# Kernel tuning notes

Hardware: AMD Instinct MI355X
Metric: run time of the kernel (lower is better)

## Reference

```python
import jax, jax.numpy as jnp
import numpy as np

D_MODEL = 1024
NUM_HEADS = 16
HEAD_DIM = D_MODEL // NUM_HEADS


def setup_inputs() -> dict:
    key = jax.random.key(0)
    k_x, k_wqkv, k_bqkv, k_wo, k_bo = jax.random.split(key, 5)
    B, T = 4, 2048
    s = 1.0 / np.sqrt(D_MODEL)
    return {
        "x": jax.random.normal(k_x, (B, T, D_MODEL), dtype=jnp.float32),
        "w_qkv": jax.random.uniform(k_wqkv, (D_MODEL, 3 * D_MODEL), jnp.float32, -s, s),
        "b_qkv": jax.random.uniform(k_bqkv, (3 * D_MODEL,), jnp.float32, -s, s),
        "w_out": jax.random.uniform(k_wo, (D_MODEL, D_MODEL), jnp.float32, -s, s),
        "b_out": jax.random.uniform(k_bo, (D_MODEL,), jnp.float32, -s, s),
    }


def reference(x, w_qkv, b_qkv, w_out, b_out):
    B, T, _ = x.shape
    H, Dh = NUM_HEADS, HEAD_DIM
    scale = Dh ** -0.5
    qkv = x @ w_qkv + b_qkv                       # [B,T,3D]
    qkv = qkv.reshape(B, T, 3, H, Dh)
    q = jnp.transpose(qkv[:, :, 0], (0, 2, 1, 3))  # [B,H,T,Dh]
    k = jnp.transpose(qkv[:, :, 1], (0, 2, 1, 3))
    v = jnp.transpose(qkv[:, :, 2], (0, 2, 1, 3))
    scores = jnp.einsum('bhqd,bhkd->bhqk', q, k) * scale
    causal = jnp.tril(jnp.ones((T, T), dtype=bool))
    scores = jnp.where(causal, scores, -jnp.inf)
    w = jax.nn.softmax(scores, axis=-1)
    out = jnp.einsum('bhqk,bhkd->bhqd', w, v)     # [B,H,T,Dh]
    out = jnp.transpose(out, (0, 2, 1, 3)).reshape(B, T, H * Dh)
    return out @ w_out + b_out
```

## Files before the change

kernel.cpp:

```cpp
#include <hip/hip_runtime.h>

typedef unsigned short u16;
typedef unsigned u32;
typedef float f32x4 __attribute__((ext_vector_type(4)));
typedef __bf16 bf16x8 __attribute__((ext_vector_type(8)));
typedef __bf16 bf16x2 __attribute__((ext_vector_type(2)));
typedef u32 u32x4 __attribute__((ext_vector_type(4)));
typedef u16 u16x4 __attribute__((ext_vector_type(4)));
typedef int i32x2 __attribute__((ext_vector_type(2)));

#define MFMA_16x16x32(a, b, c) __builtin_amdgcn_mfma_f32_16x16x32_bf16((a), (b), (c), 0, 0, 0)

#if __has_builtin(__builtin_amdgcn_exp2f)
#define EXP2(x) __builtin_amdgcn_exp2f(x)
#else
#define EXP2(x) exp2f(x)
#endif


__device__ __forceinline__ u16 f2bf(float f) {
  unsigned u = __builtin_bit_cast(unsigned, f);
  unsigned r = ((u >> 16) & 1u) + 0x7FFFu;
  return (u16)((u + r) >> 16);
}

__device__ __forceinline__ u32 pk2(float x, float y) {
  bf16x2 v = {(__bf16)x, (__bf16)y};
  return __builtin_bit_cast(u32, v);
}

__device__ __forceinline__ void gload16(const void* g, void* l) {
  __builtin_amdgcn_global_load_lds(
      (const __attribute__((address_space(1))) void*)g,
      (__attribute__((address_space(3))) void*)l, 16, 0, 0);
}



__global__ void cvt_to_bf16(const float* __restrict__ in, u16* __restrict__ out, int n) {
  const int s = blockIdx.x * 256 + threadIdx.x;
  if (s * 8 >= n) return;
  const int l = s & 63, f = (s >> 6) & 7, kb = (s >> 9) & 31, R = s >> 14;
  const int rr = ((f >> 2) << 6) + ((f & 3) << 4) + (l & 15);
  const int row = (R << 7) + rr;
  const int k = (kb << 5) + ((l >> 4) << 3);
  const float* src = in + (size_t)row * 1024 + k;
  const f32x4 a = *(const f32x4*)src;
  const f32x4 b = *(const f32x4*)(src + 4);
  u16x4 u0, u1;
#pragma unroll
  for (int j = 0; j < 4; ++j) { u0[j] = f2bf(a[j]); u1[j] = f2bf(b[j]); }
  *(u16x4*)(out + (size_t)s * 8) = u0;
  *(u16x4*)(out + (size_t)s * 8 + 4) = u1;
}

__global__ void transpose_cvt(const float* __restrict__ in, u16* __restrict__ out,
                              int rows, int cols) {
  __shared__ float t[64][65];
  const int rb = blockIdx.y * 64, cb = blockIdx.x * 64;
  for (int i = threadIdx.x; i < 4096; i += 256) {
    const int r = i >> 6, c = i & 63;
    t[r][c] = in[(size_t)(rb + r) * cols + cb + c];
  }
  __syncthreads();
  for (int u = threadIdx.x; u < 512; u += 256) {
    const int c = u >> 3, k8 = u & 7;
    const int nrow = cb + c;
    const int kg = rb + k8 * 8;
    const int R = nrow >> 7, rr = nrow & 127;
    const int fB = ((rr >> 6) << 2) + ((rr >> 4) & 3);
    const int kb = kg >> 5, koct = (kg >> 3) & 3;
    u16* dst = out + (((size_t)R * 32 + kb) * 8 + fB) * 512 + ((koct << 4) + (rr & 15)) * 8;
    u16x4 u0, u1;
#pragma unroll
    for (int j = 0; j < 4; ++j) {
      u0[j] = f2bf(t[k8 * 8 + j][c]);
      u1[j] = f2bf(t[k8 * 8 + 4 + j][c]);
    }
    *(u16x4*)dst = u0;
    *(u16x4*)(dst + 4) = u1;
  }
}

template <int EPI>
__global__ __launch_bounds__(256, 4) void gemm_bt(
    const u16* __restrict__ A, const u16* __restrict__ Bt, int K,
    const float* __restrict__ bias,
    u16* __restrict__ oq, u16* __restrict__ ok, u16* __restrict__ ov,
    float* __restrict__ of, int N, int nbx) {
  __shared__ __align__(16) u16 As[8192];
  __shared__ __align__(16) u16 Bs[8192];
  const int tid = threadIdx.x;
  const int lane = tid & 63, w = tid >> 6;
  const int g = lane >> 4, cc = lane & 15;
  const int wr = w >> 1, wc = w & 1;

  const int cpx = gridDim.x >> 3;
  const int bid = ((int)blockIdx.x & 7) * cpx + ((int)blockIdx.x >> 3);
  const int bx = bid % nbx, by = bid / nbx;

  const u16* pa = A + ((size_t)by * 256 + w) * 512 + lane * 8;
  const u16* pb = Bt + ((size_t)bx * 256 + w) * 512 + lane * 8;

  u16* la0 = &As[w * 512 + lane * 8];
  u16* lb0 = &Bs[w * 512 + lane * 8];
  const u16* ard = &As[(wr * 4) * 512 + lane * 8];
  const u16* brd = &Bs[(wc * 4) * 512 + lane * 8];

  f32x4 acc[4][4] = {};

  const int ns = K >> 6;
  for (int s = 0; s < ns; ++s) {
    const size_t o = (size_t)s * 8192;
    gload16(pa + o, la0);
    gload16(pa + o + 2048, la0 + 2048);
    gload16(pa + o + 4096, la0 + 4096);
    gload16(pa + o + 6144, la0 + 6144);
    gload16(pb + o, lb0);
    gload16(pb + o + 2048, lb0 + 2048);
    gload16(pb + o + 4096, lb0 + 4096);
    gload16(pb + o + 6144, lb0 + 6144);
    __syncthreads();
#pragma unroll
    for (int kk = 0; kk < 2; ++kk) {
      bf16x8 af[4], bf[4];
#pragma unroll
      for (int mi = 0; mi < 4; ++mi) af[mi] = *(const bf16x8*)(ard + kk * 4096 + mi * 512);
#pragma unroll
      for (int ni = 0; ni < 4; ++ni) bf[ni] = *(const bf16x8*)(brd + kk * 4096 + ni * 512);
      __builtin_amdgcn_s_setprio(1);
#pragma unroll
      for (int mi = 0; mi < 4; ++mi)
#pragma unroll
        for (int ni = 0; ni < 4; ++ni)
          acc[mi][ni] = MFMA_16x16x32(af[mi], bf[ni], acc[mi][ni]);
      __builtin_amdgcn_s_setprio(0);
    }
    __syncthreads();
  }

  const int m00 = by * 128 + wr * 64 + 4 * g;
  const int n00 = bx * 128 + wc * 64;
#pragma unroll
  for (int ni = 0; ni < 4; ++ni) {
    const int n = n00 + ni * 16 + cc;
    const float bn = bias[n];
    if constexpr (EPI == 0) {
      const int which = n >> 10;
      const int d = n & 1023;
      const int h = d >> 6, dh = d & 63;
      const int dcf = dh >> 5, gf = (dh >> 3) & 3, e = dh & 7;
      const int niv = dh >> 4, ccv = dh & 15;
#pragma unroll
      for (int mi = 0; mi < 4; ++mi) {
        const int mb = m00 + mi * 16;
        const int b = mb >> 11, t0b = mb & 2047;
        const int bh2 = b * 16 + h;
        const int kt = t0b >> 7, tr = t0b & 127;
        if (which == 2) {
          const int kk0 = (tr & ~12) | ((tr & 4) << 1) | ((tr & 8) >> 1);
          const int ko = kk0 >> 5, gv = (kk0 >> 3) & 3, ev = kk0 & 7;
          u16x4 pk;
#pragma unroll
          for (int r = 0; r < 4; ++r) pk[r] = f2bf(acc[mi][ni][r] + bn);
          *(u16x4*)&ov[(((size_t)bh2 * 16 + kt) * 16 + ko * 4 + niv) * 512 +
                       ((gv << 4) + ccv) * 8 + ev] = pk;
        } else if (which == 1) {
          const int ki = tr >> 4;
          u16* dst = ok + (((size_t)bh2 * 16 + kt) * 16 + dcf * 8 + ki) * 512 +
                     ((gf << 4) + (tr & 15)) * 8 + e;
#pragma unroll
          for (int r = 0; r < 4; ++r) dst[r * 8] = f2bf(acc[mi][ni][r] + bn);
        } else {
          const int wf = tr >> 5, mif = (tr >> 4) & 1;
          u16* dst = oq + (((size_t)bh2 * 16 + kt) * 16 + wf * 4 + mif * 2 + dcf) * 512 +
                     ((gf << 4) + (tr & 15)) * 8 + e;
#pragma unroll
          for (int r = 0; r < 4; ++r) dst[r * 8] = f2bf(acc[mi][ni][r] + bn);
        }
      }
    } else {
#pragma unroll
      for (int mi = 0; mi < 4; ++mi) {
        const int m = m00 + mi * 16;
#pragma unroll
        for (int r = 0; r < 4; ++r) of[(size_t)(m + r) * N + n] = acc[mi][ni][r] + bn;
      }
    }
  }
}

__global__ __launch_bounds__(256, 3) void flash_attn(
    const u16* __restrict__ Qb, const u16* __restrict__ Kb,
    const u16* __restrict__ Vt, u16* __restrict__ Ob) {
  __shared__ __align__(16) u16 Ks[8192];
  __shared__ __align__(16) u16 Vs[8192];

  const int bid = blockIdx.x;
  const int tq4 = bid >> 6, t0 = tq4 & 3, ti = tq4 >> 2;
  const int qt = (ti == 0) ? 15 - t0 : (ti == 1) ? 8 + t0 : (ti == 2) ? 7 - t0 : t0;
  const int bh = bid & 63;
  const int tid = threadIdx.x;
  const int lane = tid & 63, w = tid >> 6;
  const int g = lane >> 4, cc = lane & 15;
  const int q0 = qt * 128 + w * 32;

  bf16x8 bq[2][2];
  {
    const u16* qp = Qb + (((size_t)bh * 16 + qt) * 16 + w * 4) * 512 + lane * 8;
#pragma unroll
    for (int mi = 0; mi < 2; ++mi)
#pragma unroll
      for (int dc = 0; dc < 2; ++dc)
        bq[mi][dc] = *(const bf16x8*)(qp + (mi * 2 + dc) * 512);
  }

  const char* kp = (const char*)Kb + (size_t)bh * 262144 + w * 1024 + lane * 16;
  const char* vp = (const char*)Vt + (size_t)bh * 262144 + w * 1024 + lane * 16;
  u16* kl[4];
  u16* vl[4];
#pragma unroll
  for (int i = 0; i < 4; ++i) {
    kl[i] = &Ks[(i * 4 + w) * 512 + lane * 8];
    vl[i] = &Vs[(i * 4 + w) * 512 + lane * 8];
  }
  const u16* krd = &Ks[lane * 8];
  const u16* vrd = &Vs[lane * 8];

  const u32x4 ones_u = {0x3F803F80u, 0x3F803F80u, 0x3F803F80u, 0x3F803F80u};
  const bf16x8 ones = __builtin_bit_cast(bf16x8, ones_u);

  f32x4 acc[2][4] = {};
  f32x4 lsum[2] = {};
  float m_run[2] = {-1e30f, -1e30f};
  const float sc = 0.18033688011112042f;

  u32x4 kreg[4], vreg[4];
#pragma unroll
  for (int i = 0; i < 4; ++i) {
    kreg[i] = *(const u32x4*)(kp + i * 4096);
    vreg[i] = *(const u32x4*)(vp + i * 4096);
  }
  kp += 16384;
  vp += 16384;

  for (int kt = 0; kt <= qt; ++kt) {
    __syncthreads();
#pragma unroll
    for (int i = 0; i < 4; ++i) {
      *(u32x4*)kl[i] = kreg[i];
      *(u32x4*)vl[i] = vreg[i];
    }
    if (kt < qt) {
#pragma unroll
      for (int i = 0; i < 4; ++i) {
        kreg[i] = *(const u32x4*)(kp + i * 4096);
        vreg[i] = *(const u32x4*)(vp + i * 4096);
      }
      kp += 16384;
      vp += 16384;
    }
    __syncthreads();

#pragma unroll
    for (int mi = 0; mi < 2; ++mi) {
      f32x4 s[8] = {};
      __builtin_amdgcn_s_setprio(1);
#pragma unroll
      for (int dc = 0; dc < 2; ++dc) {
        const bf16x8 qf = bq[mi][dc];
#pragma unroll
        for (int ki = 0; ki < 8; ++ki) {
          const bf16x8 ak = *(const bf16x8*)(krd + (dc * 8 + ki) * 512);
          s[ki] = MFMA_16x16x32(ak, qf, s[ki]);
        }
      }
      __builtin_amdgcn_s_setprio(0);

      if (kt == qt) {
        const int qq = w * 32 + mi * 16 + cc;
#pragma unroll
        for (int ki = 0; ki < 8; ++ki) {
          const int kb_ = ki * 16 + 4 * g;
#pragma unroll
          for (int r = 0; r < 4; ++r)
            if (kb_ + r > qq) s[ki][r] = -1e30f;
        }
      }

      float mx = fmaxf(fmaxf(s[0][0], s[0][1]), fmaxf(s[0][2], s[0][3]));
#pragma unroll
      for (int ki = 1; ki < 8; ++ki)
        mx = fmaxf(mx, fmaxf(fmaxf(s[ki][0], s[ki][1]), fmaxf(s[ki][2], s[ki][3])));
      mx = fmaxf(mx, __shfl_xor(mx, 16));
      mx = fmaxf(mx, __shfl_xor(mx, 32));
      const float pm = mx * sc;

      if (!__all(pm - m_run[mi] <= 8.f)) {
        const float mn = fmaxf(m_run[mi], pm);
        const float sf = EXP2(m_run[mi] - mn);
        m_run[mi] = mn;
        float sfr[4];
#pragma unroll
        for (int r = 0; r < 4; ++r) sfr[r] = __shfl(sf, (lane & 48) + 4 * g + r);
#pragma unroll
        for (int r = 0; r < 4; ++r) lsum[mi][r] *= sfr[r];
#pragma unroll
        for (int ni = 0; ni < 4; ++ni)
#pragma unroll
          for (int r = 0; r < 4; ++r) acc[mi][ni][r] *= sfr[r];
      }
      const float mcur = m_run[mi];

#pragma unroll
      for (int ko = 0; ko < 4; ++ko) {
        f32x4 pe, po;
#pragma unroll
        for (int r = 0; r < 4; ++r) {
          pe[r] = EXP2(__builtin_fmaf(s[2 * ko][r], sc, -mcur));
          po[r] = EXP2(__builtin_fmaf(s[2 * ko + 1][r], sc, -mcur));
        }
        const u32 aw = pk2(pe[0], pe[1]), bw2 = pk2(pe[2], pe[3]);
        const u32 cw = pk2(po[0], po[1]), dw = pk2(po[2], po[3]);
#if __has_builtin(__builtin_amdgcn_permlane32_swap)
        const i32x2 s1 = __builtin_amdgcn_permlane32_swap((int)aw, (int)cw, false, false);
        const i32x2 s2 = __builtin_amdgcn_permlane32_swap((int)bw2, (int)dw, false, false);
        const u32x4 wv = {(u32)s1[0], (u32)s2[0], (u32)s1[1], (u32)s2[1]};
#else
        const bool lo2 = (g < 2);
        const u32 r_ac = __shfl_xor(lo2 ? cw : aw, 32);
        const u32 r_bd = __shfl_xor(lo2 ? dw : bw2, 32);
        const u32x4 wv = {lo2 ? aw : r_ac, lo2 ? bw2 : r_bd,
                          lo2 ? r_ac : cw, lo2 ? r_bd : dw};
#endif
        const bf16x8 pf = __builtin_bit_cast(bf16x8, wv);
        __builtin_amdgcn_s_setprio(1);
#pragma unroll
        for (int ni = 0; ni < 4; ++ni) {
          const bf16x8 bv = *(const bf16x8*)(vrd + (ko * 4 + ni) * 512);
          acc[mi][ni] = MFMA_16x16x32(pf, bv, acc[mi][ni]);
        }
        lsum[mi] = MFMA_16x16x32(pf, ones, lsum[mi]);
        __builtin_amdgcn_s_setprio(0);
      }
    }
  }

  const int b = bh >> 4, h = bh & 15;
#pragma unroll
  for (int mi = 0; mi < 2; ++mi) {
    f32x4 inv;
#pragma unroll
    for (int r = 0; r < 4; ++r) inv[r] = 1.f / lsum[mi][r];
#pragma unroll
    for (int ni = 0; ni < 4; ++ni) {
      const int d = h * 64 + ni * 16 + cc;
      const int kbA = d >> 5, koA = (d >> 3) & 3, eA = d & 7;
#pragma unroll
      for (int r = 0; r < 4; ++r) {
        const int tq = q0 + mi * 16 + 4 * g + r;
        const int row = b * 2048 + tq;
        const int R = row >> 7, rr = row & 127;
        const int fA = ((rr >> 6) << 2) + ((rr >> 4) & 3);
        Ob[(((size_t)R * 32 + kbA) * 8 + fA) * 512 + ((koA << 4) + (rr & 15)) * 8 + eA] =
            f2bf(acc[mi][ni][r] * inv[r]);
      }
    }
  }
}


extern "C" void kernel_launch(void* const* d_in, const int* in_sizes, int n_in,
                              void* d_out, int out_size, void* d_ws, size_t ws_size,
                              hipStream_t stream) {
  const float* x     = (const float*)d_in[0];
  const float* w_qkv = (const float*)d_in[1];
  const float* b_qkv = (const float*)d_in[2];
  const float* w_out = (const float*)d_in[3];
  const float* b_out = (const float*)d_in[4];
  float* out = (float*)d_out;
  char* ws = (char*)d_ws;

  u16* xb    = (u16*)(ws + 0);
  u16* wqkvT = (u16*)(ws + 16777216);
  u16* woutT = (u16*)(ws + 23068672);
  u16* qbuf  = (u16*)(ws + 25165824);
  u16* kbuf  = (u16*)(ws + 41943040);
  u16* vbuf  = (u16*)(ws + 58720256);

  cvt_to_bf16<<<4096, 256, 0, stream>>>(x, xb, 8388608);
  transpose_cvt<<<dim3(48, 16), 256, 0, stream>>>(w_qkv, wqkvT, 1024, 3072);
  transpose_cvt<<<dim3(16, 16), 256, 0, stream>>>(w_out, woutT, 1024, 1024);
  gemm_bt<0><<<24 * 64, 256, 0, stream>>>(xb, wqkvT, 1024, b_qkv,
                                          qbuf, kbuf, vbuf, nullptr, 3072, 24);
  flash_attn<<<1024, 256, 0, stream>>>(qbuf, kbuf, vbuf, xb);
  gemm_bt<1><<<8 * 64, 256, 0, stream>>>(xb, woutT, 1024, b_out,
                                         nullptr, nullptr, nullptr, out, 1024, 8);
}
```

Before: 157.3 us.

## Double-buffer GEMM LDS tiles and overlap next-stage loads with MFMA

```diff
diff --git a/kernel.cpp b/kernel.cpp
--- a/kernel.cpp
+++ b/kernel.cpp
@@ -88,8 +88,8 @@
     const float* __restrict__ bias,
     u16* __restrict__ oq, u16* __restrict__ ok, u16* __restrict__ ov,
     float* __restrict__ of, int N, int nbx) {
-  __shared__ __align__(16) u16 As[8192];
-  __shared__ __align__(16) u16 Bs[8192];
+  __shared__ __align__(16) u16 As[2][4096];
+  __shared__ __align__(16) u16 Bs[2][4096];
   const int tid = threadIdx.x;
   const int lane = tid & 63, w = tid >> 6;
   const int g = lane >> 4, cc = lane & 15;
@@ -102,42 +102,48 @@
   const u16* pa = A + ((size_t)by * 256 + w) * 512 + lane * 8;
   const u16* pb = Bt + ((size_t)bx * 256 + w) * 512 + lane * 8;
 
-  u16* la0 = &As[w * 512 + lane * 8];
-  u16* lb0 = &Bs[w * 512 + lane * 8];
-  const u16* ard = &As[(wr * 4) * 512 + lane * 8];
-  const u16* brd = &Bs[(wc * 4) * 512 + lane * 8];
-
   f32x4 acc[4][4] = {};
 
-  const int ns = K >> 6;
-  for (int s = 0; s < ns; ++s) {
-    const size_t o = (size_t)s * 8192;
-    gload16(pa + o, la0);
-    gload16(pa + o + 2048, la0 + 2048);
-    gload16(pa + o + 4096, la0 + 4096);
-    gload16(pa + o + 6144, la0 + 6144);
-    gload16(pb + o, lb0);
-    gload16(pb + o + 2048, lb0 + 2048);
-    gload16(pb + o + 4096, lb0 + 4096);
-    gload16(pb + o + 6144, lb0 + 6144);
+#define STG(S, T)                                              \
+  do {                                                         \
+    const size_t o_ = (size_t)(T) * 4096;                      \
+    gload16(pa + o_, &As[S][w * 512 + lane * 8]);              \
+    gload16(pa + o_ + 2048, &As[S][(w + 4) * 512 + lane * 8]); \
+    gload16(pb + o_, &Bs[S][w * 512 + lane * 8]);              \
+    gload16(pb + o_ + 2048, &Bs[S][(w + 4) * 512 + lane * 8]); \
+  } while (0)
+
+#define CMP(S, DOSTG, T)                                                 \
+  do {                                                                   \
+    bf16x8 af[4], bf[4];                                                 \
+    _Pragma("unroll") for (int mi = 0; mi < 4; ++mi)                     \
+        af[mi] = *(const bf16x8*)&As[S][(wr * 4 + mi) * 512 + lane * 8]; \
+    _Pragma("unroll") for (int ni = 0; ni < 4; ++ni)                     \
+        bf[ni] = *(const bf16x8*)&Bs[S][(wc * 4 + ni) * 512 + lane * 8]; \
+    if (DOSTG) STG(S ^ 1, T);                                            \
+    __builtin_amdgcn_s_setprio(1);                                       \
+    _Pragma("unroll") for (int mi = 0; mi < 4; ++mi)                     \
+      _Pragma("unroll") for (int ni = 0; ni < 4; ++ni)                   \
+          acc[mi][ni] = MFMA_16x16x32(af[mi], bf[ni], acc[mi][ni]);      \
+    __builtin_amdgcn_s_setprio(0);                                       \
+  } while (0)
+
+  STG(0, 0);
+  __syncthreads();
+
+  const int np = (K >> 5) >> 1;
+  for (int p = 0; p < np - 1; ++p) {
+    CMP(0, true, 2 * p + 1);
     __syncthreads();
-#pragma unroll
-    for (int kk = 0; kk < 2; ++kk) {
-      bf16x8 af[4], bf[4];
-#pragma unroll
-      for (int mi = 0; mi < 4; ++mi) af[mi] = *(const bf16x8*)(ard + kk * 4096 + mi * 512);
-#pragma unroll
-      for (int ni = 0; ni < 4; ++ni) bf[ni] = *(const bf16x8*)(brd + kk * 4096 + ni * 512);
-      __builtin_amdgcn_s_setprio(1);
-#pragma unroll
-      for (int mi = 0; mi < 4; ++mi)
-#pragma unroll
-        for (int ni = 0; ni < 4; ++ni)
-          acc[mi][ni] = MFMA_16x16x32(af[mi], bf[ni], acc[mi][ni]);
-      __builtin_amdgcn_s_setprio(0);
-    }
+    CMP(1, true, 2 * p + 2);
     __syncthreads();
   }
+  CMP(0, true, 2 * np - 1);
+  __syncthreads();
+  CMP(1, false, 0);
+
+#undef STG
+#undef CMP
 
   const int m00 = by * 128 + wr * 64 + 4 * g;
   const int n00 = bx * 128 + wc * 64;
@@ -288,10 +294,12 @@
         }
       }
 
-      float mx = fmaxf(fmaxf(s[0][0], s[0][1]), fmaxf(s[0][2], s[0][3]));
-#pragma unroll
-      for (int ki = 1; ki < 8; ++ki)
-        mx = fmaxf(mx, fmaxf(fmaxf(s[ki][0], s[ki][1]), fmaxf(s[ki][2], s[ki][3])));
+      float t4[8];
+#pragma unroll
+      for (int ki = 0; ki < 8; ++ki)
+        t4[ki] = fmaxf(fmaxf(s[ki][0], s[ki][1]), fmaxf(s[ki][2], s[ki][3]));
+      float mx = fmaxf(fmaxf(fmaxf(t4[0], t4[1]), fmaxf(t4[2], t4[3])),
+                       fmaxf(fmaxf(t4[4], t4[5]), fmaxf(t4[6], t4[7])));
       mx = fmaxf(mx, __shfl_xor(mx, 16));
       mx = fmaxf(mx, __shfl_xor(mx, 32));
       const float pm = mx * sc;
```

Result: no change. 157.4 us (+0.1%).
